# Optimization experiments

Hardware: AMD Instinct MI355X
Metric: run time of the kernel (lower is better)

## Reference

```python
import jax, jax.numpy as jnp
import numpy as np

H = 1024           # hidden_size
E = 8              # num_experts
I = 4096 // E      # expert_intermediate_size = 512
V = 32000          # vocab_size
T = 4096           # num_tokens


def setup_inputs() -> dict:
    key = jax.random.key(0)
    ks = jax.random.split(key, 6)
    x = jax.random.normal(ks[0], (T, H), dtype=jnp.float32)
    token_ids = jax.random.randint(ks[1], (T,), 0, V, dtype=jnp.int64)
    mu = jax.random.normal(ks[2], (T, H), dtype=jnp.float32)
    # learned parameters (kaiming-like scale)
    gate_up_proj = jax.random.normal(ks[3], (E, H, 2 * I), dtype=jnp.float32) * (1.0 / np.sqrt(H))
    down_proj = jax.random.normal(ks[4], (E, I, H), dtype=jnp.float32) * (1.0 / np.sqrt(I))
    mu_w = jax.random.normal(ks[5], (E, H), dtype=jnp.float32) * 0.02  # mu_router.weight [E, H]
    return {"x": x, "token_ids": token_ids, "mu": mu,
            "gate_up_proj": gate_up_proj, "down_proj": down_proj, "mu_w": mu_w}


def reference(x, token_ids, mu, gate_up_proj, down_proj, mu_w):
    # deterministic base routing: expert = token_id % num_experts
    tid = jnp.clip(token_ids, 0, V - 1)
    base_expert = tid % E                                   # [T]
    # mu router biases the routing decision
    mu_logits = mu @ mu_w.T                                 # [T, E]
    combined = jax.nn.one_hot(base_expert, E, dtype=jnp.float32) * 10.0 + mu_logits
    expert_ids = jnp.argmax(combined, axis=-1)              # [T]

    out = jnp.zeros_like(x)
    # fixed small loop over experts; rows not routed to e are discarded by the mask,
    # so computing the dense GEMM over all tokens gives identical selected rows.
    for e in range(E):
        mask = (expert_ids == e)                            # [T]
        gu = x @ gate_up_proj[e]                            # [T, 2I]
        gate, up = gu[:, :I], gu[:, I:]
        inter = jax.nn.silu(gate) * up                      # [T, I]
        y = inter @ down_proj[e]                            # [T, H]
        out = jnp.where(mask[:, None], y, out)
    return out
```

## Files before the change

### kernel.cpp

```cpp
#include <hip/hip_runtime.h>
#include <cmath>

constexpr int T_DIM = 4096;
constexpr int H_DIM = 1024;
constexpr int E_DIM = 8;
constexpr int I_DIM = 512;
constexpr int V_DIM = 32000;

typedef _Float16 half_t;
typedef __attribute__((ext_vector_type(8))) _Float16 halfx8;
typedef __attribute__((ext_vector_type(4))) _Float16 halfx4;
typedef __attribute__((ext_vector_type(4))) float floatx4;

#define GLOAD16(g, l)                                                        \
    __builtin_amdgcn_global_load_lds(                                        \
        (const __attribute__((address_space(1))) void*)(g),                  \
        (__attribute__((address_space(3))) void*)(l), 16, 0, 0)

constexpr int  CNT_STRIDE  = 16;
constexpr size_t OFF_COUNTS = 0;
constexpr size_t OFF_EID    = 1024;
constexpr size_t OFF_TOKL   = OFF_EID + (size_t)T_DIM * 4;
constexpr size_t OFF_XB     = OFF_TOKL + (size_t)E_DIM * T_DIM * 4;
constexpr size_t OFF_GUPT   = OFF_XB + (size_t)T_DIM * H_DIM * 2;
constexpr size_t OFF_DOWNT  = OFF_GUPT + (size_t)E_DIM * 2 * I_DIM * H_DIM * 2;
constexpr size_t OFF_INTER  = OFF_DOWNT + (size_t)E_DIM * H_DIM * I_DIM * 2;

__global__ __launch_bounds__(256) void prep_kernel(
    const float* __restrict__ x, const float* __restrict__ gup,
    const float* __restrict__ mu, const int* __restrict__ token_ids,
    const float* __restrict__ mu_w, half_t* __restrict__ xb,
    half_t* __restrict__ gupT, int* __restrict__ expert_id)
{
    const int z = blockIdx.z, bx = blockIdx.x, by = blockIdx.y;
    const int tid = threadIdx.x;

    if (z >= 2) {
        const int t = ((z - 2) * 256 + by) * 8 + bx;

        const float4 m = *(const float4*)&mu[(size_t)t * H_DIM + tid * 4];
        float acc[E_DIM];
#pragma unroll
        for (int e = 0; e < E_DIM; ++e) {
            const float4 w = *(const float4*)&mu_w[e * H_DIM + tid * 4];
            acc[e] = m.x * w.x + m.y * w.y + m.z * w.z + m.w * w.w;
        }
#pragma unroll
        for (int e = 0; e < E_DIM; ++e) {
#pragma unroll
            for (int off = 32; off > 0; off >>= 1)
                acc[e] += __shfl_down(acc[e], off, 64);
        }
        __shared__ float part[4][E_DIM];
        const int lane = tid & 63, w = tid >> 6;
        if (lane == 0) {
#pragma unroll
            for (int e = 0; e < E_DIM; ++e) part[w][e] = acc[e];
        }
        __syncthreads();
        if (tid == 0) {
            int tk = token_ids[t];
            tk = min(max(tk, 0), V_DIM - 1);
            const int be = tk & (E_DIM - 1);
            float best = -1e30f; int bi = 0;
#pragma unroll
            for (int e = 0; e < E_DIM; ++e) {
                const float c = part[0][e] + part[1][e] + part[2][e] + part[3][e]
                              + (e == be ? 10.f : 0.f);
                if (c > best) { best = c; bi = e; }
            }
            expert_id[t] = bi;
        }
        return;
    }

    if (z == 1) {
        const int idx = by * 8 + bx;
        if (idx >= 512) return;
#pragma unroll
        for (int p = 0; p < 4; ++p) {
            const size_t i = (size_t)idx * 8192 + p * 2048 + tid * 8;
            const float4 v0 = *(const float4*)&x[i];
            const float4 v1 = *(const float4*)&x[i + 4];
            halfx8 h = { (half_t)v0.x, (half_t)v0.y, (half_t)v0.z, (half_t)v0.w,
                         (half_t)v1.x, (half_t)v1.y, (half_t)v1.z, (half_t)v1.w };
            *(halfx8*)&xb[i] = h;
        }
        return;
    }

    __shared__ float tile[64][65];
    const float* se = gup + (size_t)bx * H_DIM * (2 * I_DIM);
    half_t* de = gupT + (size_t)bx * (2 * I_DIM) * H_DIM;
    constexpr int N = 1024, K = H_DIM;
    const int n0 = (by & 15) * 64, k0 = (by >> 4) * 64;
    const int c4 = (tid & 15) * 4, r0 = tid >> 4;
#pragma unroll
    for (int p = 0; p < 4; ++p) {
        const int r = r0 + p * 16;
        const float4 v = *(const float4*)&se[(size_t)(k0 + r) * N + n0 + c4];
        tile[r][c4 + 0] = v.x; tile[r][c4 + 1] = v.y;
        tile[r][c4 + 2] = v.z; tile[r][c4 + 3] = v.w;
    }
    __syncthreads();
#pragma unroll
    for (int p = 0; p < 4; ++p) {
        const int n = r0 + p * 16;
        const int kc = c4;
        halfx4 h = { (half_t)tile[kc + 0][n], (half_t)tile[kc + 1][n],
                     (half_t)tile[kc + 2][n], (half_t)tile[kc + 3][n] };
        *(halfx4*)&de[(size_t)(n0 + n) * K + k0 + kc] = h;
    }
}

__global__ __launch_bounds__(1024) void scatter_kernel(
    const int* __restrict__ expert_id, int* __restrict__ counts,
    int* __restrict__ tok_list)
{
    const int e = blockIdx.x;
    const int tid = threadIdx.x;
    const int lane = tid & 63, wv = tid >> 6;
    __shared__ int wcnt[16];
    int base = 0;
#pragma unroll
    for (int r = 0; r < 4; ++r) {
        const int t = r * 1024 + tid;
        const bool m = (expert_id[t] == e);
        const unsigned long long mask = __ballot(m);
        const int wrank = (int)__popcll(mask & ((1ull << lane) - 1ull));
        if (lane == 0) wcnt[wv] = (int)__popcll(mask);
        __syncthreads();
        int pre = 0, tot = 0;
#pragma unroll
        for (int i = 0; i < 16; ++i) {
            const int c = wcnt[i];
            pre += (i < wv) ? c : 0;
            tot += c;
        }
        if (m) tok_list[e * T_DIM + base + pre + wrank] = t;
        base += tot;
        __syncthreads();
    }
    if (tid == 0) counts[e * CNT_STRIDE] = base;
}

__global__ __launch_bounds__(256) void gemm1_mfma_kernel(
    const half_t* __restrict__ xb, const half_t* __restrict__ gupT,
    const float* __restrict__ down, half_t* __restrict__ downT,
    const int* __restrict__ counts, const int* __restrict__ tok_list,
    half_t* __restrict__ inter)
{
    __shared__ __align__(16) char smraw[64 * 64 * 2 + 128 * 64 * 2 + 64 * 4];
    const int tid = threadIdx.x;
    const int e = blockIdx.x;

    if (blockIdx.z >= 64) {
        float (*tile)[65] = (float (*)[65])smraw;
        const float* se = down + (size_t)e * I_DIM * H_DIM;
        half_t* de = downT + (size_t)e * H_DIM * I_DIM;
        const int n0 = (blockIdx.z - 64) * 64, k0 = blockIdx.y * 64;
        const int c4 = (tid & 15) * 4, r0 = tid >> 4;
#pragma unroll
        for (int p = 0; p < 4; ++p) {
            const int r = r0 + p * 16;
            const float4 v = *(const float4*)&se[(size_t)(k0 + r) * H_DIM + n0 + c4];
            tile[r][c4 + 0] = v.x; tile[r][c4 + 1] = v.y;
            tile[r][c4 + 2] = v.z; tile[r][c4 + 3] = v.w;
        }
        __syncthreads();
#pragma unroll
        for (int p = 0; p < 4; ++p) {
            const int n = r0 + p * 16;
            const int kc = c4;
            halfx4 h = { (half_t)tile[kc + 0][n], (half_t)tile[kc + 1][n],
                         (half_t)tile[kc + 2][n], (half_t)tile[kc + 3][n] };
            *(halfx4*)&de[(size_t)(n0 + n) * I_DIM + k0 + kc] = h;
        }
        return;
    }

    const int count = counts[e * CNT_STRIDE];
    const int m0 = blockIdx.z * 64;
    if (m0 >= count) return;
    const int n0 = blockIdx.y * 64;

    half_t* const As = (half_t*)smraw;
    half_t* const Bs = (half_t*)(smraw + 64 * 64 * 2);
    int* const toks = (int*)(smraw + 64 * 64 * 2 + 128 * 64 * 2);

    if (tid < 64) {
        const int m = m0 + tid;
        toks[tid] = (m < count) ? tok_list[e * T_DIM + m] : -1;
    }
    __syncthreads();

    const half_t* We = gupT + (size_t)e * (2 * I_DIM) * H_DIM;

    const int lane = tid & 63;
    const int w = tid >> 6;
    const int lr = lane >> 3, lc = lane & 7;

    const half_t* aptr[2]; const half_t* bptr[4];
    half_t *alds[2], *blds[4];
#pragma unroll
    for (int j = 0; j < 2; ++j) {
        const int r = w * 16 + j * 8 + lr;
        const int cg = lc ^ (r & 7);
        const int tk = toks[r];
        aptr[j] = xb + (size_t)(tk < 0 ? 0 : tk) * H_DIM + cg * 8;
        alds[j] = &As[(w * 16 + j * 8) * 64];
    }
#pragma unroll
    for (int j = 0; j < 4; ++j) {
        const int n = w * 32 + j * 8 + lr;
        const int col = (n < 64) ? (n0 + n) : (I_DIM + n0 + (n - 64));
        const int cg = lc ^ (n & 7);
        bptr[j] = We + (size_t)col * H_DIM + cg * 8;
        blds[j] = &Bs[(w * 32 + j * 8) * 64];
    }

    const floatx4 fzero = {0.f, 0.f, 0.f, 0.f};
    floatx4 accg[2][2], accu[2][2];
#pragma unroll
    for (int i = 0; i < 2; ++i)
#pragma unroll
        for (int j = 0; j < 2; ++j) { accg[i][j] = fzero; accu[i][j] = fzero; }

    const int wr = w >> 1, wc = w & 1;
    const int fm = lane & 15, q = lane >> 4;
    const int fm7 = fm & 7;

    for (int k0 = 0; k0 < H_DIM; k0 += 64) {
#pragma unroll
        for (int j = 0; j < 2; ++j) GLOAD16(aptr[j] + k0, alds[j]);
#pragma unroll
        for (int j = 0; j < 4; ++j) GLOAD16(bptr[j] + k0, blds[j]);
        __syncthreads();

#pragma unroll
        for (int ks = 0; ks < 2; ++ks) {
            const int swz = ((ks * 4 + q) ^ fm7) * 8;
            const halfx8 a0 = *(const halfx8*)&As[(32 * wr + fm) * 64 + swz];
            const halfx8 a1 = *(const halfx8*)&As[(32 * wr + 16 + fm) * 64 + swz];
#pragma unroll
            for (int ct = 0; ct < 2; ++ct) {
                const int ng = wc * 32 + ct * 16 + fm;
                const halfx8 bg = *(const halfx8*)&Bs[ng * 64 + swz];
                const halfx8 bu = *(const halfx8*)&Bs[(64 + ng) * 64 + swz];
                accg[0][ct] = __builtin_amdgcn_mfma_f32_16x16x32_f16(a0, bg, accg[0][ct], 0, 0, 0);
                accg[1][ct] = __builtin_amdgcn_mfma_f32_16x16x32_f16(a1, bg, accg[1][ct], 0, 0, 0);
                accu[0][ct] = __builtin_amdgcn_mfma_f32_16x16x32_f16(a0, bu, accu[0][ct], 0, 0, 0);
                accu[1][ct] = __builtin_amdgcn_mfma_f32_16x16x32_f16(a1, bu, accu[1][ct], 0, 0, 0);
            }
        }
        __syncthreads();
    }

#pragma unroll
    for (int rt = 0; rt < 2; ++rt)
#pragma unroll
        for (int r = 0; r < 4; ++r) {
            const int row = 32 * wr + 16 * rt + q * 4 + r;
            const int tk = toks[row];
            if (tk < 0) continue;
#pragma unroll
            for (int ct = 0; ct < 2; ++ct) {
                const float g = accg[rt][ct][r];
                const float u = accu[rt][ct][r];
                const float s = g / (1.f + __expf(-g)) * u;
                inter[(size_t)tk * I_DIM + n0 + wc * 32 + ct * 16 + fm] = (half_t)s;
            }
        }
}

__global__ __launch_bounds__(256) void gemm2_mfma_kernel(
    const half_t* __restrict__ inter, const half_t* __restrict__ downT,
    const int* __restrict__ counts, const int* __restrict__ tok_list,
    float* __restrict__ out)
{
    const int e = blockIdx.x;
    const int count = counts[e * CNT_STRIDE];
    const int m0 = blockIdx.z * 64;
    if (m0 >= count) return;
    const int n0 = blockIdx.y * 128;

    __shared__ __align__(16) half_t As[64 * 64];
    __shared__ __align__(16) half_t Bs[128 * 64];
    __shared__ int toks[64];

    const int tid = threadIdx.x;
    if (tid < 64) {
        const int m = m0 + tid;
        toks[tid] = (m < count) ? tok_list[e * T_DIM + m] : -1;
    }
    __syncthreads();

    const half_t* De = downT + (size_t)e * H_DIM * I_DIM;

    const int lane = tid & 63;
    const int w = tid >> 6;
    const int lr = lane >> 3, lc = lane & 7;

    const half_t* aptr[2]; const half_t* bptr[4];
    half_t *alds[2], *blds[4];
#pragma unroll
    for (int j = 0; j < 2; ++j) {
        const int r = w * 16 + j * 8 + lr;
        const int cg = lc ^ (r & 7);
        const int tk = toks[r];
        aptr[j] = inter + (size_t)(tk < 0 ? 0 : tk) * I_DIM + cg * 8;
        alds[j] = &As[(w * 16 + j * 8) * 64];
    }
#pragma unroll
    for (int j = 0; j < 4; ++j) {
        const int n = w * 32 + j * 8 + lr;
        const int cg = lc ^ (n & 7);
        bptr[j] = De + (size_t)(n0 + n) * I_DIM + cg * 8;
        blds[j] = &Bs[(w * 32 + j * 8) * 64];
    }

    const floatx4 fzero = {0.f, 0.f, 0.f, 0.f};
    floatx4 acc[2][4];
#pragma unroll
    for (int i = 0; i < 2; ++i)
#pragma unroll
        for (int j = 0; j < 4; ++j) acc[i][j] = fzero;

    const int wr = w >> 1, wc = w & 1;
    const int fm = lane & 15, q = lane >> 4;
    const int fm7 = fm & 7;

    for (int k0 = 0; k0 < I_DIM; k0 += 64) {
#pragma unroll
        for (int j = 0; j < 2; ++j) GLOAD16(aptr[j] + k0, alds[j]);
#pragma unroll
        for (int j = 0; j < 4; ++j) GLOAD16(bptr[j] + k0, blds[j]);
        __syncthreads();

#pragma unroll
        for (int ks = 0; ks < 2; ++ks) {
            const int swz = ((ks * 4 + q) ^ fm7) * 8;
            const halfx8 a0 = *(const halfx8*)&As[(32 * wr + fm) * 64 + swz];
            const halfx8 a1 = *(const halfx8*)&As[(32 * wr + 16 + fm) * 64 + swz];
#pragma unroll
            for (int ct = 0; ct < 4; ++ct) {
                const halfx8 b = *(const halfx8*)&Bs[(wc * 64 + ct * 16 + fm) * 64 + swz];
                acc[0][ct] = __builtin_amdgcn_mfma_f32_16x16x32_f16(a0, b, acc[0][ct], 0, 0, 0);
                acc[1][ct] = __builtin_amdgcn_mfma_f32_16x16x32_f16(a1, b, acc[1][ct], 0, 0, 0);
            }
        }
        __syncthreads();
    }

#pragma unroll
    for (int rt = 0; rt < 2; ++rt)
#pragma unroll
        for (int r = 0; r < 4; ++r) {
            const int row = 32 * wr + 16 * rt + q * 4 + r;
            const int tk = toks[row];
            if (tk < 0) continue;
#pragma unroll
            for (int ct = 0; ct < 4; ++ct)
                out[(size_t)tk * H_DIM + n0 + wc * 64 + ct * 16 + fm] = acc[rt][ct][r];
        }
}

extern "C" void kernel_launch(void* const* d_in, const int* in_sizes, int n_in,
                              void* d_out, int out_size, void* d_ws, size_t ws_size,
                              hipStream_t stream)
{
    const float* x         = (const float*)d_in[0];
    const int*   token_ids = (const int*)  d_in[1];
    const float* mu        = (const float*)d_in[2];
    const float* down      = (const float*)d_in[4];
    const float* gup       = (const float*)d_in[3];
    const float* mu_w      = (const float*)d_in[5];
    float* out = (float*)d_out;

    char* ws = (char*)d_ws;
    int*    counts    = (int*)(ws + OFF_COUNTS);
    int*    expert_id = (int*)(ws + OFF_EID);
    int*    tok_list  = (int*)(ws + OFF_TOKL);
    half_t* xb        = (half_t*)(ws + OFF_XB);
    half_t* gupT      = (half_t*)(ws + OFF_GUPT);
    half_t* downT     = (half_t*)(ws + OFF_DOWNT);
    half_t* inter     = (half_t*)(ws + OFF_INTER);

    prep_kernel<<<dim3(8, 256, 4), 256, 0, stream>>>(
        x, gup, mu, token_ids, mu_w, xb, gupT, expert_id);
    scatter_kernel<<<E_DIM, 1024, 0, stream>>>(expert_id, counts, tok_list);
    gemm1_mfma_kernel<<<dim3(E_DIM, 8, 80), 256, 0, stream>>>(
        xb, gupT, down, downT, counts, tok_list, inter);
    gemm2_mfma_kernel<<<dim3(E_DIM, 8, T_DIM / 64), 256, 0, stream>>>(
        inter, downT, counts, tok_list, out);
}
```

Before: 158.6 us.

## Double-buffer LDS tiles in both expert GEMM kernels to overlap loads with MFMA

Both grouped GEMM kernels now use two LDS buffers for A and B tiles. The next k-slice is fetched with global_load_lds while MFMAs run on the current slice, so there is one barrier per step instead of two. This aims to hide global memory latency behind compute. LDS per block grows to about 48KB, which may cut occupancy, and correctness relies on the barrier placement covering the async direct-to-LDS loads.

```diff
diff --git a/kernel.cpp b/kernel.cpp
--- a/kernel.cpp
+++ b/kernel.cpp
@@ -150,7 +150,7 @@
     const int* __restrict__ counts, const int* __restrict__ tok_list,
     half_t* __restrict__ inter)
 {
-    __shared__ __align__(16) char smraw[64 * 64 * 2 + 128 * 64 * 2 + 64 * 4];
+    __shared__ __align__(16) char smraw[49152 + 64 * 4];
     const int tid = threadIdx.x;
     const int e = blockIdx.x;
 
@@ -184,9 +184,11 @@
     if (m0 >= count) return;
     const int n0 = blockIdx.y * 64;
 
-    half_t* const As = (half_t*)smraw;
-    half_t* const Bs = (half_t*)(smraw + 64 * 64 * 2);
-    int* const toks = (int*)(smraw + 64 * 64 * 2 + 128 * 64 * 2);
+    half_t* const As0 = (half_t*)smraw;
+    half_t* const As1 = (half_t*)(smraw + 8192);
+    half_t* const Bs0 = (half_t*)(smraw + 16384);
+    half_t* const Bs1 = (half_t*)(smraw + 32768);
+    int* const toks = (int*)(smraw + 49152);
 
     if (tid < 64) {
         const int m = m0 + tid;
@@ -201,14 +203,15 @@
     const int lr = lane >> 3, lc = lane & 7;
 
     const half_t* aptr[2]; const half_t* bptr[4];
-    half_t *alds[2], *blds[4];
+    half_t *a0l[2], *a1l[2], *b0l[4], *b1l[4];
 #pragma unroll
     for (int j = 0; j < 2; ++j) {
         const int r = w * 16 + j * 8 + lr;
         const int cg = lc ^ (r & 7);
         const int tk = toks[r];
         aptr[j] = xb + (size_t)(tk < 0 ? 0 : tk) * H_DIM + cg * 8;
-        alds[j] = &As[(w * 16 + j * 8) * 64];
+        const int off = (w * 16 + j * 8) * 64;
+        a0l[j] = As0 + off; a1l[j] = As1 + off;
     }
 #pragma unroll
     for (int j = 0; j < 4; ++j) {
@@ -216,7 +219,8 @@
         const int col = (n < 64) ? (n0 + n) : (I_DIM + n0 + (n - 64));
         const int cg = lc ^ (n & 7);
         bptr[j] = We + (size_t)col * H_DIM + cg * 8;
-        blds[j] = &Bs[(w * 32 + j * 8) * 64];
+        const int off = (w * 32 + j * 8) * 64;
+        b0l[j] = Bs0 + off; b1l[j] = Bs1 + off;
     }
 
     const floatx4 fzero = {0.f, 0.f, 0.f, 0.f};
@@ -230,29 +234,49 @@
     const int fm = lane & 15, q = lane >> 4;
     const int fm7 = fm & 7;
 
-    for (int k0 = 0; k0 < H_DIM; k0 += 64) {
-#pragma unroll
-        for (int j = 0; j < 2; ++j) GLOAD16(aptr[j] + k0, alds[j]);
-#pragma unroll
-        for (int j = 0; j < 4; ++j) GLOAD16(bptr[j] + k0, blds[j]);
-        __syncthreads();
-
+    auto mfma_phase = [&](const half_t* A_, const half_t* B_) {
 #pragma unroll
         for (int ks = 0; ks < 2; ++ks) {
             const int swz = ((ks * 4 + q) ^ fm7) * 8;
-            const halfx8 a0 = *(const halfx8*)&As[(32 * wr + fm) * 64 + swz];
-            const halfx8 a1 = *(const halfx8*)&As[(32 * wr + 16 + fm) * 64 + swz];
+            const halfx8 a0 = *(const halfx8*)&A_[(32 * wr + fm) * 64 + swz];
+            const halfx8 a1 = *(const halfx8*)&A_[(32 * wr + 16 + fm) * 64 + swz];
 #pragma unroll
             for (int ct = 0; ct < 2; ++ct) {
                 const int ng = wc * 32 + ct * 16 + fm;
-                const halfx8 bg = *(const halfx8*)&Bs[ng * 64 + swz];
-                const halfx8 bu = *(const halfx8*)&Bs[(64 + ng) * 64 + swz];
+                const halfx8 bg = *(const halfx8*)&B_[ng * 64 + swz];
+                const halfx8 bu = *(const halfx8*)&B_[(64 + ng) * 64 + swz];
                 accg[0][ct] = __builtin_amdgcn_mfma_f32_16x16x32_f16(a0, bg, accg[0][ct], 0, 0, 0);
                 accg[1][ct] = __builtin_amdgcn_mfma_f32_16x16x32_f16(a1, bg, accg[1][ct], 0, 0, 0);
                 accu[0][ct] = __builtin_amdgcn_mfma_f32_16x16x32_f16(a0, bu, accu[0][ct], 0, 0, 0);
                 accu[1][ct] = __builtin_amdgcn_mfma_f32_16x16x32_f16(a1, bu, accu[1][ct], 0, 0, 0);
             }
         }
+    };
+
+#pragma unroll
+    for (int j = 0; j < 2; ++j) GLOAD16(aptr[j], a0l[j]);
+#pragma unroll
+    for (int j = 0; j < 4; ++j) GLOAD16(bptr[j], b0l[j]);
+    __syncthreads();
+
+    for (int it = 0; it < H_DIM / 64; it += 2) {
+        const int k1 = (it + 1) * 64;
+        if (k1 < H_DIM) {
+#pragma unroll
+            for (int j = 0; j < 2; ++j) GLOAD16(aptr[j] + k1, a1l[j]);
+#pragma unroll
+            for (int j = 0; j < 4; ++j) GLOAD16(bptr[j] + k1, b1l[j]);
+        }
+        mfma_phase(As0, Bs0);
+        __syncthreads();
+        const int k2 = (it + 2) * 64;
+        if (k2 < H_DIM) {
+#pragma unroll
+            for (int j = 0; j < 2; ++j) GLOAD16(aptr[j] + k2, a0l[j]);
+#pragma unroll
+            for (int j = 0; j < 4; ++j) GLOAD16(bptr[j] + k2, b0l[j]);
+        }
+        mfma_phase(As1, Bs1);
         __syncthreads();
     }
 
@@ -284,9 +308,12 @@
     if (m0 >= count) return;
     const int n0 = blockIdx.y * 128;
 
-    __shared__ __align__(16) half_t As[64 * 64];
-    __shared__ __align__(16) half_t Bs[128 * 64];
-    __shared__ int toks[64];
+    __shared__ __align__(16) char smraw[49152 + 64 * 4];
+    half_t* const As0 = (half_t*)smraw;
+    half_t* const As1 = (half_t*)(smraw + 8192);
+    half_t* const Bs0 = (half_t*)(smraw + 16384);
+    half_t* const Bs1 = (half_t*)(smraw + 32768);
+    int* const toks = (int*)(smraw + 49152);
 
     const int tid = threadIdx.x;
     if (tid < 64) {
@@ -302,21 +329,23 @@
     const int lr = lane >> 3, lc = lane & 7;
 
     const half_t* aptr[2]; const half_t* bptr[4];
-    half_t *alds[2], *blds[4];
+    half_t *a0l[2], *a1l[2], *b0l[4], *b1l[4];
 #pragma unroll
     for (int j = 0; j < 2; ++j) {
         const int r = w * 16 + j * 8 + lr;
         const int cg = lc ^ (r & 7);
         const int tk = toks[r];
         aptr[j] = inter + (size_t)(tk < 0 ? 0 : tk) * I_DIM + cg * 8;
-        alds[j] = &As[(w * 16 + j * 8) * 64];
+        const int off = (w * 16 + j * 8) * 64;
+        a0l[j] = As0 + off; a1l[j] = As1 + off;
     }
 #pragma unroll
     for (int j = 0; j < 4; ++j) {
         const int n = w * 32 + j * 8 + lr;
         const int cg = lc ^ (n & 7);
         bptr[j] = De + (size_t)(n0 + n) * I_DIM + cg * 8;
-        blds[j] = &Bs[(w * 32 + j * 8) * 64];
+        const int off = (w * 32 + j * 8) * 64;
+        b0l[j] = Bs0 + off; b1l[j] = Bs1 + off;
     }
 
     const floatx4 fzero = {0.f, 0.f, 0.f, 0.f};
@@ -330,25 +359,45 @@
     const int fm = lane & 15, q = lane >> 4;
     const int fm7 = fm & 7;
 
-    for (int k0 = 0; k0 < I_DIM; k0 += 64) {
-#pragma unroll
-        for (int j = 0; j < 2; ++j) GLOAD16(aptr[j] + k0, alds[j]);
-#pragma unroll
-        for (int j = 0; j < 4; ++j) GLOAD16(bptr[j] + k0, blds[j]);
-        __syncthreads();
-
+    auto mfma_phase = [&](const half_t* A_, const half_t* B_) {
 #pragma unroll
         for (int ks = 0; ks < 2; ++ks) {
             const int swz = ((ks * 4 + q) ^ fm7) * 8;
-            const halfx8 a0 = *(const halfx8*)&As[(32 * wr + fm) * 64 + swz];
-            const halfx8 a1 = *(const halfx8*)&As[(32 * wr + 16 + fm) * 64 + swz];
+            const halfx8 a0 = *(const halfx8*)&A_[(32 * wr + fm) * 64 + swz];
+            const halfx8 a1 = *(const halfx8*)&A_[(32 * wr + 16 + fm) * 64 + swz];
 #pragma unroll
             for (int ct = 0; ct < 4; ++ct) {
-                const halfx8 b = *(const halfx8*)&Bs[(wc * 64 + ct * 16 + fm) * 64 + swz];
+                const halfx8 b = *(const halfx8*)&B_[(wc * 64 + ct * 16 + fm) * 64 + swz];
                 acc[0][ct] = __builtin_amdgcn_mfma_f32_16x16x32_f16(a0, b, acc[0][ct], 0, 0, 0);
                 acc[1][ct] = __builtin_amdgcn_mfma_f32_16x16x32_f16(a1, b, acc[1][ct], 0, 0, 0);
             }
         }
+    };
+
+#pragma unroll
+    for (int j = 0; j < 2; ++j) GLOAD16(aptr[j], a0l[j]);
+#pragma unroll
+    for (int j = 0; j < 4; ++j) GLOAD16(bptr[j], b0l[j]);
+    __syncthreads();
+
+    for (int it = 0; it < I_DIM / 64; it += 2) {
+        const int k1 = (it + 1) * 64;
+        if (k1 < I_DIM) {
+#pragma unroll
+            for (int j = 0; j < 2; ++j) GLOAD16(aptr[j] + k1, a1l[j]);
+#pragma unroll
+            for (int j = 0; j < 4; ++j) GLOAD16(bptr[j] + k1, b1l[j]);
+        }
+        mfma_phase(As0, Bs0);
+        __syncthreads();
+        const int k2 = (it + 2) * 64;
+        if (k2 < I_DIM) {
+#pragma unroll
+            for (int j = 0; j < 2; ++j) GLOAD16(aptr[j] + k2, a0l[j]);
+#pragma unroll
+            for (int j = 0; j < 4; ++j) GLOAD16(bptr[j] + k2, b0l[j]);
+        }
+        mfma_phase(As1, Bs1);
         __syncthreads();
     }
 
@@ -372,8 +421,8 @@
     const float* x         = (const float*)d_in[0];
     const int*   token_ids = (const int*)  d_in[1];
     const float* mu        = (const float*)d_in[2];
+    const float* gup       = (const float*)d_in[3];
     const float* down      = (const float*)d_in[4];
-    const float* gup       = (const float*)d_in[3];
     const float* mu_w      = (const float*)d_in[5];
     float* out = (float*)d_out;
 
```

Result: no change. 156.7 us (-1.2%).
